# Performance work log

Measured on AMD Instinct MI355X. Metric: run time of the kernel, lower is better.

The kernel has to match this reference:

```python
import jax, jax.numpy as jnp
import numpy as np

NA, NP_, E = 40000, 60000, 80000
D, H = 512, 8
DK = D // H
SQRT_DK = float(DK) ** 0.5


def setup_inputs() -> dict:
    key = jax.random.key(0)
    ks = list(jax.random.split(key, 20))
    it = iter(ks)

    def nrm(shape, scale=1.0):
        return jax.random.normal(next(it), shape, dtype=jnp.float32) * scale

    xav = (6.0 / (DK + DK)) ** 0.5  # xavier_uniform bound for (dk, dk)
    w_scale = D ** -0.5
    inp = {
        "h_author": nrm((NA, D)),
        "h_paper": nrm((NP_, D)),
        "writes_src": jax.random.randint(next(it), (E,), 0, NA, dtype=jnp.int32),
        "writes_dst": jax.random.randint(next(it), (E,), 0, NP_, dtype=jnp.int32),
        "cites_src": jax.random.randint(next(it), (E,), 0, NP_, dtype=jnp.int32),
        "cites_dst": jax.random.randint(next(it), (E,), 0, NP_, dtype=jnp.int32),
        "wb_src": jax.random.randint(next(it), (E,), 0, NP_, dtype=jnp.int32),
        "wb_dst": jax.random.randint(next(it), (E,), 0, NA, dtype=jnp.int32),
        # per-node-type linear weights (2 types: 0=author, 1=paper)
        "Wk": nrm((2, D, D), w_scale), "bk": jnp.zeros((2, D), jnp.float32),
        "Wq": nrm((2, D, D), w_scale), "bq": jnp.zeros((2, D), jnp.float32),
        "Wv": nrm((2, D, D), w_scale), "bv": jnp.zeros((2, D), jnp.float32),
        "Wa": nrm((2, D, D), w_scale), "ba": jnp.zeros((2, D), jnp.float32),
        # per-relation params (3 relations: 0=writes, 1=cites, 2=written_by)
        "rel_att": jax.random.uniform(next(it), (3, H, DK, DK), jnp.float32, -xav, xav),
        "rel_msg": jax.random.uniform(next(it), (3, H, DK, DK), jnp.float32, -xav, xav),
        "rel_pri": jnp.ones((3, H), jnp.float32),
        "skip": jnp.ones((2,), jnp.float32),
    }
    return inp


def _edge_attn_agg(k, q, v, src, dst, pri, n_dst):
    # k, v: (N_src, H, DK) relation-transformed; q: (N_dst, H, DK)
    s = jnp.einsum('ehd,ehd->eh', q[dst], k[src]) * pri / SQRT_DK  # (E, H)
    m = jax.ops.segment_max(s, dst, num_segments=n_dst)            # edge softmax by dst
    ex = jnp.exp(s - m[dst])
    den = jax.ops.segment_sum(ex, dst, num_segments=n_dst)
    a = ex / den[dst]
    return jax.ops.segment_sum(v[src] * a[:, :, None], dst, num_segments=n_dst)


def reference(h_author, h_paper, writes_src, writes_dst, cites_src, cites_dst,
              wb_src, wb_dst, Wk, bk, Wq, bq, Wv, bv, Wa, ba,
              rel_att, rel_msg, rel_pri, skip):
    def proj(h, W, b, t):
        return (h @ W[t] + b[t]).reshape(-1, H, DK)

    k_a, v_a, q_a = proj(h_author, Wk, bk, 0), proj(h_author, Wv, bv, 0), proj(h_author, Wq, bq, 0)
    k_p, v_p, q_p = proj(h_paper, Wk, bk, 1), proj(h_paper, Wv, bv, 1), proj(h_paper, Wq, bq, 1)

    def rel(k, v, r):
        return (jnp.einsum('nhd,hde->nhe', k, rel_att[r]),
                jnp.einsum('nhd,hde->nhe', v, rel_msg[r]))

    k0, v0 = rel(k_a, v_a, 0)  # writes: author -> paper
    agg_w = _edge_attn_agg(k0, q_p, v0, writes_src, writes_dst, rel_pri[0], NP_)
    k1, v1 = rel(k_p, v_p, 1)  # cites: paper -> paper
    agg_c = _edge_attn_agg(k1, q_p, v1, cites_src, cites_dst, rel_pri[1], NP_)
    k2, v2 = rel(k_p, v_p, 2)  # written_by: paper -> author
    agg_b = _edge_attn_agg(k2, q_a, v2, wb_src, wb_dst, rel_pri[2], NA)

    t_paper = ((agg_w + agg_c) * 0.5).reshape(NP_, D)  # cross_reducer='mean'
    t_author = agg_b.reshape(NA, D)

    alpha = jax.nn.sigmoid(skip)
    out_a = (t_author @ Wa[0] + ba[0]) * alpha[0] + h_author * (1.0 - alpha[0])
    out_p = (t_paper @ Wa[1] + ba[1]) * alpha[1] + h_paper * (1.0 - alpha[1])
    return out_a, out_p
```

## Files before the change

kernel.cpp:

```cpp
#include <hip/hip_runtime.h>
#include <math.h>

#define D_ 512
#define H_ 8

typedef short bf16x8 __attribute__((ext_vector_type(8)));
typedef float f32x4 __attribute__((ext_vector_type(4)));

__device__ __forceinline__ unsigned short f2bf(float x) {
  unsigned int u = __float_as_uint(x);
  unsigned int r = (u + 0x7fff + ((u >> 16) & 1)) >> 16;
  return (unsigned short)r;
}
__device__ __forceinline__ float bf2f(unsigned short b) {
  return __uint_as_float(((unsigned int)b) << 16);
}

struct PrepArgs {
  const float *hA, *hP;
  unsigned short *hA16, *hP16;
  const float *fWin[6], *fbin[6], *frel[6];
  unsigned short *fWf[6];
  float *fbf[6];
  const float *tW[4];
  unsigned short *tWt[4];
  const float *cin[2];
  float *cout[2];
  int *degree;
  int NT;
  int b1, b2, b3, b4, b5;
};

__global__ __launch_bounds__(512) void prep_kernel(PrepArgs p) {
  const int b = blockIdx.x, t = threadIdx.x;
  if (b < p.b2) {
    const float* in; unsigned short* out; long i;
    if (b < p.b1) { in = p.hA; out = p.hA16; i = (long)b * 512 + t; }
    else          { in = p.hP; out = p.hP16; i = (long)(b - p.b1) * 512 + t; }
    float4 a = ((const float4*)in)[i * 2];
    float4 c = ((const float4*)in)[i * 2 + 1];
    bf16x8 o;
    o[0] = (short)f2bf(a.x); o[1] = (short)f2bf(a.y);
    o[2] = (short)f2bf(a.z); o[3] = (short)f2bf(a.w);
    o[4] = (short)f2bf(c.x); o[5] = (short)f2bf(c.y);
    o[6] = (short)f2bf(c.z); o[7] = (short)f2bf(c.w);
    ((bf16x8*)out)[i] = o;
  } else if (b < p.b3) {
    int idx = b - p.b2;
    int job = idx / 513, row = idx - job * 513;
    int h = t >> 6, e = t & 63;
    const float* src = (row < D_) ? (p.fWin[job] + (long)row * D_) : p.fbin[job];
    const float* rl = p.frel[job] + h * 64 * 64;
    float acc = 0.f;
#pragma unroll 16
    for (int d = 0; d < 64; ++d)
      acc = fmaf(src[h * 64 + d], rl[d * 64 + e], acc);
    if (row < D_) p.fWf[job][(long)t * D_ + row] = f2bf(acc);
    else p.fbf[job][t] = acc;
  } else if (b < p.b4) {
    int idx = b - p.b3;
    int job = idx >> 9, n = idx & 511;
    p.tWt[job][(long)n * D_ + t] = f2bf(p.tW[job][(long)t * D_ + n]);
  } else if (b < p.b5) {
    int job = b - p.b4;
    p.cout[job][t] = p.cin[job][t];
  } else {
    int i = (b - p.b5) * 512 + t;
    if (i < p.NT) p.degree[i] = 0;
  }
}

__global__ void hist_kernel(const int* __restrict__ w_dst,
                            const int* __restrict__ c_dst,
                            const int* __restrict__ b_dst,
                            int* __restrict__ degree, int E, int NP) {
  int i = blockIdx.x * blockDim.x + threadIdx.x;
  if (i >= 3 * E) return;
  int r = i / E, e = i - r * E;
  int d, base;
  if (r == 0)      { d = w_dst[e]; base = 0; }
  else if (r == 1) { d = c_dst[e]; base = NP; }
  else             { d = b_dst[e]; base = 2 * NP; }
  atomicAdd(degree + base + d, 1);
}

__global__ void scan1_kernel(const int* __restrict__ in, int* __restrict__ out,
                             int* __restrict__ aux, int n) {
  __shared__ int tmp[256];
  int t = threadIdx.x;
  int i = blockIdx.x * 256 + t;
  int v = (i < n) ? in[i] : 0;
  tmp[t] = v;
  __syncthreads();
#pragma unroll
  for (int d = 1; d < 256; d <<= 1) {
    int add = (t >= d) ? tmp[t - d] : 0;
    __syncthreads();
    tmp[t] += add;
    __syncthreads();
  }
  if (i < n) out[i] = tmp[t] - v;
  if (t == 255) aux[blockIdx.x] = tmp[255];
}

__global__ void scan2_kernel(int* __restrict__ aux, int nb) {
  __shared__ int tmp[1024];
  int t = threadIdx.x;
  int v = (t < nb) ? aux[t] : 0;
  tmp[t] = v;
  __syncthreads();
#pragma unroll
  for (int d = 1; d < 1024; d <<= 1) {
    int add = (t >= d) ? tmp[t - d] : 0;
    __syncthreads();
    tmp[t] += add;
    __syncthreads();
  }
  if (t < nb) aux[t] = tmp[t] - v;
}

__global__ void scan3_kernel(int* __restrict__ starts, int* __restrict__ cursor,
                             const int* __restrict__ aux, int n) {
  int i = blockIdx.x * 256 + threadIdx.x;
  if (i >= n) return;
  int s = starts[i] + aux[blockIdx.x];
  starts[i] = s;
  cursor[i] = s;
}

__global__ void scatter_kernel(const int* __restrict__ w_src, const int* __restrict__ w_dst,
                               const int* __restrict__ c_src, const int* __restrict__ c_dst,
                               const int* __restrict__ b_src, const int* __restrict__ b_dst,
                               int* __restrict__ cursor, int* __restrict__ csr,
                               int E, int NP) {
  int i = blockIdx.x * blockDim.x + threadIdx.x;
  if (i >= 3 * E) return;
  int r = i / E, e = i - r * E;
  int s, d, base;
  if (r == 0)      { s = w_src[e]; d = w_dst[e]; base = 0; }
  else if (r == 1) { s = c_src[e]; d = c_dst[e]; base = NP; }
  else             { s = b_src[e]; d = b_dst[e]; base = 2 * NP; }
  int pos = atomicAdd(cursor + base + d, 1);
  csr[pos] = s;
}

__global__ __launch_bounds__(256) void attn_all(
    const unsigned short* __restrict__ Pq,
    const unsigned short* __restrict__ Akw, const unsigned short* __restrict__ Avw,
    const unsigned short* __restrict__ Pkc, const unsigned short* __restrict__ Pvc,
    const unsigned short* __restrict__ Aq,
    const unsigned short* __restrict__ Pkb, const unsigned short* __restrict__ Pvb,
    const int* __restrict__ csr, const int* __restrict__ starts,
    const int* __restrict__ degree, const float* __restrict__ pri,
    unsigned short* __restrict__ t16, int NP, int NA, int NAp) {
  long gid = (long)blockIdx.x * blockDim.x + threadIdx.x;
  int gw = (int)(gid >> 6);
  if (gw >= NP + NAp) return;
  int lane = threadIdx.x & 63;
  int h = lane >> 3, off = (lane & 7) << 3;

  const unsigned short* q;
  long orow;
  int node;
  const int paper = gw < NP;
  if (paper) {
    node = gw; q = Pq;
    orow = (long)(NAp + node) * D_ + h * 64 + off;
  } else {
    int aw = gw - NP;
    orow = (long)aw * D_ + h * 64 + off;
    if (aw >= NA) {
      bf16x8 z;
#pragma unroll
      for (int r = 0; r < 8; ++r) z[r] = 0;
      *(bf16x8*)(t16 + orow) = z;
      return;
    }
    node = aw; q = Aq;
  }

  bf16x8 qv = *(const bf16x8*)(q + (long)node * D_ + h * 64 + off);
  float qf[8];
#pragma unroll
  for (int r = 0; r < 8; ++r) qf[r] = bf2f((unsigned short)qv[r]);

  float res[8] = {};

  auto process = [&](const unsigned short* K, const unsigned short* V,
                     int nodeabs, float ps) {
    int st = starts[nodeabs], dg = degree[nodeabs];
    float m = -INFINITY, l = 0.f;
    float acc[8] = {};
    for (int i = 0; i < dg; ++i) {
      int s = csr[st + i];
      const long ro = (long)s * D_ + h * 64 + off;
      bf16x8 kv = *(const bf16x8*)(K + ro);
      bf16x8 vv = *(const bf16x8*)(V + ro);
      float dot = 0.f;
#pragma unroll
      for (int r = 0; r < 8; ++r)
        dot = fmaf(qf[r], bf2f((unsigned short)kv[r]), dot);
      dot += __shfl_xor(dot, 1);
      dot += __shfl_xor(dot, 2);
      dot += __shfl_xor(dot, 4);
      float sc = dot * ps;
      float mn = fmaxf(m, sc);
      float scale = __expf(m - mn);
      float pv = __expf(sc - mn);
      l = l * scale + pv;
#pragma unroll
      for (int r = 0; r < 8; ++r)
        acc[r] = acc[r] * scale + pv * bf2f((unsigned short)vv[r]);
      m = mn;
    }
    if (l > 0.f) {
      float inv = 1.f / l;
#pragma unroll
      for (int r = 0; r < 8; ++r) res[r] += acc[r] * inv;
    }
  };

  float outscale;
  if (paper) {
    process(Akw, Avw, node, pri[h] * 0.125f);
    process(Pkc, Pvc, NP + node, pri[8 + h] * 0.125f);
    outscale = 0.5f;
  } else {
    process(Pkb, Pvb, 2 * NP + node, pri[16 + h] * 0.125f);
    outscale = 1.0f;
  }

  bf16x8 o;
#pragma unroll
  for (int r = 0; r < 8; ++r) o[r] = (short)f2bf(res[r] * outscale);
  *(bf16x8*)(t16 + orow) = o;
}

__device__ __forceinline__ void gload_lds16(const void* g, void* l) {
  __builtin_amdgcn_global_load_lds(
      (const __attribute__((address_space(1))) void*)g,
      (__attribute__((address_space(3))) void*)l, 16, 0, 0);
}

struct ProjArgs {
  const unsigned short *A0, *A1;
  const unsigned short *B0, *B1;
  const float *bias0, *bias1;
  void* outs[8];
  int M0, M1, split;
};

__global__ __launch_bounds__(512, 2) void gemm_proj(ProjArgs pa) {
  __shared__ unsigned short Asm[2][256 * 64];
  __shared__ unsigned short Bsm[2][256 * 64];

  const int nwg = gridDim.x, orig = blockIdx.x;
  const int q8 = nwg >> 3, r8 = nwg & 7;
  const int xcd = orig & 7, pos = orig >> 3;
  const int wgid =
      (xcd < r8 ? xcd * (q8 + 1) : r8 * (q8 + 1) + (xcd - r8) * q8) + pos;

  int reg, mt, nt;
  if (wgid < pa.split) { reg = 0; mt = wgid / 6; nt = wgid - mt * 6; }
  else { int r = wgid - pa.split; reg = 1; mt = r / 10; nt = r - mt * 10; }
  const unsigned short* A  = reg ? pa.A1 : pa.A0;
  const unsigned short* Bt = reg ? pa.B1 : pa.B0;
  const float* bias = reg ? pa.bias1 : pa.bias0;
  const int M = reg ? pa.M1 : pa.M0;
  const int bm = mt * 256, bn = nt * 256;

  const int tid = threadIdx.x;
  const int wave = tid >> 6, lane = tid & 63;
  const int wm = (wave >> 2) * 128;
  const int wn = (wave & 3) * 64;
  const int srow = tid >> 3;
  const int swz = ((tid & 7) ^ (srow & 7)) * 8;

  f32x4 acc[8][4] = {};
  const int rr = lane & 15;
  const int rx = (rr & 7) << 4;

  auto STAGE = [&](int buf, int kt) {
    const int k0 = kt * 64;
#pragma unroll
    for (int i = 0; i < 4; ++i) {
      int gr = bm + srow + i * 64;
      if (gr >= M) gr = M - 1;
      gload_lds16(A + (long)gr * D_ + k0 + swz, &Asm[buf][i * 4096 + wave * 512]);
    }
#pragma unroll
    for (int i = 0; i < 4; ++i) {
      int gr = bn + srow + i * 64;
      gload_lds16(Bt + (long)gr * D_ + k0 + swz, &Bsm[buf][i * 4096 + wave * 512]);
    }
  };

  STAGE(0, 0);
  STAGE(1, 1);
#pragma unroll
  for (int t = 0; t < 8; ++t) {
    const int p = t & 1;
    if (t == 7) asm volatile("s_waitcnt vmcnt(0)" ::: "memory");
    else        asm volatile("s_waitcnt vmcnt(8)" ::: "memory");
    __builtin_amdgcn_s_barrier();
    asm volatile("" ::: "memory");

#pragma unroll
    for (int kk = 0; kk < 2; ++kk) {
      const int cb = kk * 64 + (lane >> 4) * 16;
      const int cs = cb ^ rx;
      bf16x8 af[8], bfr[4];
#pragma unroll
      for (int mi = 0; mi < 8; ++mi)
        af[mi] = *(const bf16x8*)((const char*)&Asm[p][0] +
                                  (wm + mi * 16 + rr) * 128 + cs);
#pragma unroll
      for (int nj = 0; nj < 4; ++nj)
        bfr[nj] = *(const bf16x8*)((const char*)&Bsm[p][0] +
                                   (wn + nj * 16 + rr) * 128 + cs);
      __builtin_amdgcn_s_setprio(1);
#pragma unroll
      for (int mi = 0; mi < 8; ++mi)
#pragma unroll
        for (int nj = 0; nj < 4; ++nj)
          acc[mi][nj] = __builtin_amdgcn_mfma_f32_16x16x32_bf16(
              af[mi], bfr[nj], acc[mi][nj], 0, 0, 0);
      __builtin_amdgcn_s_setprio(0);
    }

    asm volatile("" ::: "memory");
    __builtin_amdgcn_s_barrier();
    asm volatile("" ::: "memory");
    if (t + 2 < 8) STAGE(p, t + 2);
  }

  const int cr = (lane >> 4) * 4;
  const int cc = lane & 15;
  const int matu = (bn + wn) >> 9;
  const int wcb = (bn + wn) & 511;
  unsigned short* ob16 = (unsigned short*)pa.outs[(reg ? 3 : 0) + matu];
#pragma unroll
  for (int mi = 0; mi < 8; ++mi) {
    int rowb = bm + wm + mi * 16 + cr;
#pragma unroll
    for (int nj = 0; nj < 4; ++nj) {
      int col = bn + wn + nj * 16 + cc;
      float bb = bias[col];
#pragma unroll
      for (int r = 0; r < 4; ++r) {
        int row = rowb + r;
        if (row >= M) continue;
        float val = acc[mi][nj][r] + bb;
        ob16[(long)row * D_ + wcb + nj * 16 + cc] = f2bf(val);
      }
    }
  }
}

struct OutArgs {
  const unsigned short* A;
  const unsigned short *B0, *B1;
  const float *bias0, *bias1;
  const float *H0, *H1;
  const float* skip;
  float *o0, *o1;
  int mtsplit, NAp, M0, M1;
};

__global__ __launch_bounds__(512, 2) void gemm_out(OutArgs oa) {
  __shared__ unsigned short Asm[2][256 * 64];
  __shared__ unsigned short Bsm[2][256 * 64];

  const int nwg = gridDim.x, orig = blockIdx.x;
  const int q8 = nwg >> 3, r8 = nwg & 7;
  const int xcd = orig & 7, pos = orig >> 3;
  const int wgid =
      (xcd < r8 ? xcd * (q8 + 1) : r8 * (q8 + 1) + (xcd - r8) * q8) + pos;

  const int bmt = wgid >> 1;
  const int bn = (wgid & 1) * 256;
  const int reg = bmt >= oa.mtsplit;
  const int bm = (reg ? bmt - oa.mtsplit : bmt) * 256;
  const int abase = reg ? oa.NAp : 0;
  const int M = reg ? oa.M1 : oa.M0;
  const unsigned short* Bt = reg ? oa.B1 : oa.B0;
  const float* bias = reg ? oa.bias1 : oa.bias0;
  const float* Hres = reg ? oa.H1 : oa.H0;
  float* outp = reg ? oa.o1 : oa.o0;

  const int tid = threadIdx.x;
  const int wave = tid >> 6, lane = tid & 63;
  const int wm = (wave >> 2) * 128;
  const int wn = (wave & 3) * 64;
  const int srow = tid >> 3;
  const int swz = ((tid & 7) ^ (srow & 7)) * 8;

  f32x4 acc[8][4] = {};
  const int rr = lane & 15;
  const int rx = (rr & 7) << 4;

  auto STAGE = [&](int buf, int kt) {
    const int k0 = kt * 64;
#pragma unroll
    for (int i = 0; i < 4; ++i) {
      int gr = bm + srow + i * 64;
      if (gr >= M) gr = M - 1;
      gload_lds16(oa.A + (long)(abase + gr) * D_ + k0 + swz,
                  &Asm[buf][i * 4096 + wave * 512]);
    }
#pragma unroll
    for (int i = 0; i < 4; ++i) {
      int gr = bn + srow + i * 64;
      gload_lds16(Bt + (long)gr * D_ + k0 + swz,
                  &Bsm[buf][i * 4096 + wave * 512]);
    }
  };

  STAGE(0, 0);
  STAGE(1, 1);
#pragma unroll
  for (int t = 0; t < 8; ++t) {
    const int p = t & 1;
    if (t == 7) asm volatile("s_waitcnt vmcnt(0)" ::: "memory");
    else        asm volatile("s_waitcnt vmcnt(8)" ::: "memory");
    __builtin_amdgcn_s_barrier();
    asm volatile("" ::: "memory");

#pragma unroll
    for (int kk = 0; kk < 2; ++kk) {
      const int cb = kk * 64 + (lane >> 4) * 16;
      const int cs = cb ^ rx;
      bf16x8 af[8], bfr[4];
#pragma unroll
      for (int mi = 0; mi < 8; ++mi)
        af[mi] = *(const bf16x8*)((const char*)&Asm[p][0] +
                                  (wm + mi * 16 + rr) * 128 + cs);
#pragma unroll
      for (int nj = 0; nj < 4; ++nj)
        bfr[nj] = *(const bf16x8*)((const char*)&Bsm[p][0] +
                                   (wn + nj * 16 + rr) * 128 + cs);
      __builtin_amdgcn_s_setprio(1);
#pragma unroll
      for (int mi = 0; mi < 8; ++mi)
#pragma unroll
        for (int nj = 0; nj < 4; ++nj)
          acc[mi][nj] = __builtin_amdgcn_mfma_f32_16x16x32_bf16(
              af[mi], bfr[nj], acc[mi][nj], 0, 0, 0);
      __builtin_amdgcn_s_setprio(0);
    }

    asm volatile("" ::: "memory");
    __builtin_amdgcn_s_barrier();
    asm volatile("" ::: "memory");
    if (t + 2 < 8) STAGE(p, t + 2);
  }

  float sv = oa.skip[reg];
  float alpha = 1.f / (1.f + expf(-sv));
  float beta = 1.f - alpha;
  const int cr = (lane >> 4) * 4;
  const int cc = lane & 15;
#pragma unroll
  for (int mi = 0; mi < 8; ++mi) {
    int rowb = bm + wm + mi * 16 + cr;
#pragma unroll
    for (int nj = 0; nj < 4; ++nj) {
      int col = bn + wn + nj * 16 + cc;
      float bb = bias[col];
#pragma unroll
      for (int r = 0; r < 4; ++r) {
        int row = rowb + r;
        if (row >= M) continue;
        float val = acc[mi][nj][r] + bb;
        val = val * alpha + Hres[(long)row * D_ + col] * beta;
        outp[(long)row * D_ + col] = val;
      }
    }
  }
}

extern "C" void kernel_launch(void* const* d_in, const int* in_sizes, int n_in,
                              void* d_out, int out_size, void* d_ws, size_t ws_size,
                              hipStream_t stream) {
  const float* h_author = (const float*)d_in[0];
  const float* h_paper  = (const float*)d_in[1];
  const int* w_src = (const int*)d_in[2];
  const int* w_dst = (const int*)d_in[3];
  const int* c_src = (const int*)d_in[4];
  const int* c_dst = (const int*)d_in[5];
  const int* b_src = (const int*)d_in[6];
  const int* b_dst = (const int*)d_in[7];
  const float* Wk = (const float*)d_in[8];
  const float* bk = (const float*)d_in[9];
  const float* Wq = (const float*)d_in[10];
  const float* bq = (const float*)d_in[11];
  const float* Wv = (const float*)d_in[12];
  const float* bv = (const float*)d_in[13];
  const float* Wa = (const float*)d_in[14];
  const float* ba = (const float*)d_in[15];
  const float* rel_att = (const float*)d_in[16];
  const float* rel_msg = (const float*)d_in[17];
  const float* rel_pri = (const float*)d_in[18];
  const float* skip = (const float*)d_in[19];

  const int NA = in_sizes[0] / D_;
  const int NP = in_sizes[1] / D_;
  const int E  = in_sizes[2];
  const int NT = 2 * NP + NA;
  const int tA = (NA + 255) / 256;
  const int tP = (NP + 255) / 256;
  const int NAp = tA * 256;

  char* w = (char*)d_ws;
  auto alloc = [&](long bytes) {
    char* p = w;
    w += (bytes + 255) & ~255L;
    return p;
  };
  unsigned short* hA16 = (unsigned short*)alloc((long)NA * D_ * 2);
  unsigned short* hP16 = (unsigned short*)alloc((long)NP * D_ * 2);
  unsigned short* Pq   = (unsigned short*)alloc((long)NP * D_ * 2);
  unsigned short* Pkc  = (unsigned short*)alloc((long)NP * D_ * 2);
  unsigned short* Pvc  = (unsigned short*)alloc((long)NP * D_ * 2);
  unsigned short* Pkb  = (unsigned short*)alloc((long)NP * D_ * 2);
  unsigned short* Pvb  = (unsigned short*)alloc((long)NP * D_ * 2);
  unsigned short* Aq   = (unsigned short*)alloc((long)NA * D_ * 2);
  unsigned short* Akw  = (unsigned short*)alloc((long)NA * D_ * 2);
  unsigned short* Avw  = (unsigned short*)alloc((long)NA * D_ * 2);
  unsigned short* t16  = (unsigned short*)alloc((long)(NAp + NP) * D_ * 2);
  unsigned short* BtP  = (unsigned short*)alloc((long)2560 * D_ * 2);
  unsigned short* BtA  = (unsigned short*)alloc((long)1536 * D_ * 2);
  float* bfP           = (float*)alloc(2560 * 4);
  float* bfA           = (float*)alloc(1536 * 4);
  unsigned short* Wa0t = (unsigned short*)alloc((long)D_ * D_ * 2);
  unsigned short* Wa1t = (unsigned short*)alloc((long)D_ * D_ * 2);
  int* degree          = (int*)alloc((long)NT * 4);
  int* starts          = (int*)alloc((long)NT * 4);
  int* cursor          = (int*)alloc((long)NT * 4);
  int* csr             = (int*)alloc((long)3 * E * 4);
  int* aux             = (int*)alloc(((long)NT / 256 + 2) * 4);

  const long WD = (long)D_ * D_;
  const long RS = (long)H_ * 64 * 64;
  const long SEG = (long)D_ * D_;

  float* out_a = (float*)d_out;
  float* out_p = out_a + (long)NA * D_;

  {
    PrepArgs p;
    p.hA = h_author; p.hP = h_paper; p.hA16 = hA16; p.hP16 = hP16;
    p.fWin[0] = Wk + WD; p.fbin[0] = bk + D_; p.frel[0] = rel_att + RS;
    p.fWf[0] = BtP + SEG;     p.fbf[0] = bfP + 512;
    p.fWin[1] = Wv + WD; p.fbin[1] = bv + D_; p.frel[1] = rel_msg + RS;
    p.fWf[1] = BtP + 2 * SEG; p.fbf[1] = bfP + 1024;
    p.fWin[2] = Wk + WD; p.fbin[2] = bk + D_; p.frel[2] = rel_att + 2 * RS;
    p.fWf[2] = BtP + 3 * SEG; p.fbf[2] = bfP + 1536;
    p.fWin[3] = Wv + WD; p.fbin[3] = bv + D_; p.frel[3] = rel_msg + 2 * RS;
    p.fWf[3] = BtP + 4 * SEG; p.fbf[3] = bfP + 2048;
    p.fWin[4] = Wk;      p.fbin[4] = bk;      p.frel[4] = rel_att;
    p.fWf[4] = BtA + SEG;     p.fbf[4] = bfA + 512;
    p.fWin[5] = Wv;      p.fbin[5] = bv;      p.frel[5] = rel_msg;
    p.fWf[5] = BtA + 2 * SEG; p.fbf[5] = bfA + 1024;
    p.tW[0] = Wq + WD; p.tWt[0] = BtP;
    p.tW[1] = Wq;      p.tWt[1] = BtA;
    p.tW[2] = Wa;      p.tWt[2] = Wa0t;
    p.tW[3] = Wa + WD; p.tWt[3] = Wa1t;
    p.cin[0] = bq + D_; p.cout[0] = bfP;
    p.cin[1] = bq;      p.cout[1] = bfA;
    p.degree = degree; p.NT = NT;
    p.b1 = NA / 8;
    p.b2 = p.b1 + NP / 8;
    p.b3 = p.b2 + 6 * 513;
    p.b4 = p.b3 + 4 * 512;
    p.b5 = p.b4 + 2;
    int total = p.b5 + (NT + 511) / 512;
    prep_kernel<<<total, 512, 0, stream>>>(p);
  }

  {
    int th = 3 * E;
    hist_kernel<<<(th + 255) / 256, 256, 0, stream>>>(w_dst, c_dst, b_dst,
                                                      degree, E, NP);
    int nb = (NT + 255) / 256;
    scan1_kernel<<<nb, 256, 0, stream>>>(degree, starts, aux, NT);
    scan2_kernel<<<1, 1024, 0, stream>>>(aux, nb);
    scan3_kernel<<<nb, 256, 0, stream>>>(starts, cursor, aux, NT);
    scatter_kernel<<<(th + 255) / 256, 256, 0, stream>>>(
        w_src, w_dst, c_src, c_dst, b_src, b_dst, cursor, csr, E, NP);
  }

  {
    ProjArgs pa;
    pa.A0 = hA16; pa.A1 = hP16;
    pa.B0 = BtA;  pa.B1 = BtP;
    pa.bias0 = bfA; pa.bias1 = bfP;
    pa.outs[0] = Aq;  pa.outs[1] = Akw; pa.outs[2] = Avw;
    pa.outs[3] = Pq;  pa.outs[4] = Pkc; pa.outs[5] = Pvc;
    pa.outs[6] = Pkb; pa.outs[7] = Pvb;
    pa.M0 = NA; pa.M1 = NP;
    pa.split = tA * 6;
    int nwg = pa.split + tP * 10;
    gemm_proj<<<nwg, 512, 0, stream>>>(pa);
  }

  {
    long th = (long)(NP + NAp) * 64;
    attn_all<<<(int)((th + 255) / 256), 256, 0, stream>>>(
        Pq, Akw, Avw, Pkc, Pvc, Aq, Pkb, Pvb,
        csr, starts, degree, rel_pri, t16, NP, NA, NAp);
  }

  {
    OutArgs oa;
    oa.A = t16;
    oa.B0 = Wa0t; oa.B1 = Wa1t;
    oa.bias0 = ba; oa.bias1 = ba + D_;
    oa.H0 = h_author; oa.H1 = h_paper;
    oa.skip = skip;
    oa.o0 = out_a; oa.o1 = out_p;
    oa.mtsplit = tA; oa.NAp = NAp; oa.M0 = NA; oa.M1 = NP;
    int nwg = (tA + tP) * 2;
    gemm_out<<<nwg, 512, 0, stream>>>(oa);
  }
}
```

Before: 919.0 us.

## Shrink GEMM tiles to 256x128 with triple-buffered LDS and split staging

Both GEMM kernels (projection and output) now use 256x128 tiles instead of 256x256. Each wave computes a 64x64 sub-tile, which halves the accumulator registers. LDS staging goes from double to triple buffering, and each prefetch is split into two halves issued between the kk sub-steps, so global loads overlap the MFMA work more evenly. The launch grids double to match. The intent is better occupancy and latency hiding. The cost is more B-tile and A-tile re-reads across workgroups, plus an extra barrier per k-step.

```diff
diff --git a/kernel.cpp b/kernel.cpp
--- a/kernel.cpp
+++ b/kernel.cpp
@@ -250,113 +250,6 @@
   int M0, M1, split;
 };
 
-__global__ __launch_bounds__(512, 2) void gemm_proj(ProjArgs pa) {
-  __shared__ unsigned short Asm[2][256 * 64];
-  __shared__ unsigned short Bsm[2][256 * 64];
-
-  const int nwg = gridDim.x, orig = blockIdx.x;
-  const int q8 = nwg >> 3, r8 = nwg & 7;
-  const int xcd = orig & 7, pos = orig >> 3;
-  const int wgid =
-      (xcd < r8 ? xcd * (q8 + 1) : r8 * (q8 + 1) + (xcd - r8) * q8) + pos;
-
-  int reg, mt, nt;
-  if (wgid < pa.split) { reg = 0; mt = wgid / 6; nt = wgid - mt * 6; }
-  else { int r = wgid - pa.split; reg = 1; mt = r / 10; nt = r - mt * 10; }
-  const unsigned short* A  = reg ? pa.A1 : pa.A0;
-  const unsigned short* Bt = reg ? pa.B1 : pa.B0;
-  const float* bias = reg ? pa.bias1 : pa.bias0;
-  const int M = reg ? pa.M1 : pa.M0;
-  const int bm = mt * 256, bn = nt * 256;
-
-  const int tid = threadIdx.x;
-  const int wave = tid >> 6, lane = tid & 63;
-  const int wm = (wave >> 2) * 128;
-  const int wn = (wave & 3) * 64;
-  const int srow = tid >> 3;
-  const int swz = ((tid & 7) ^ (srow & 7)) * 8;
-
-  f32x4 acc[8][4] = {};
-  const int rr = lane & 15;
-  const int rx = (rr & 7) << 4;
-
-  auto STAGE = [&](int buf, int kt) {
-    const int k0 = kt * 64;
-#pragma unroll
-    for (int i = 0; i < 4; ++i) {
-      int gr = bm + srow + i * 64;
-      if (gr >= M) gr = M - 1;
-      gload_lds16(A + (long)gr * D_ + k0 + swz, &Asm[buf][i * 4096 + wave * 512]);
-    }
-#pragma unroll
-    for (int i = 0; i < 4; ++i) {
-      int gr = bn + srow + i * 64;
-      gload_lds16(Bt + (long)gr * D_ + k0 + swz, &Bsm[buf][i * 4096 + wave * 512]);
-    }
-  };
-
-  STAGE(0, 0);
-  STAGE(1, 1);
-#pragma unroll
-  for (int t = 0; t < 8; ++t) {
-    const int p = t & 1;
-    if (t == 7) asm volatile("s_waitcnt vmcnt(0)" ::: "memory");
-    else        asm volatile("s_waitcnt vmcnt(8)" ::: "memory");
-    __builtin_amdgcn_s_barrier();
-    asm volatile("" ::: "memory");
-
-#pragma unroll
-    for (int kk = 0; kk < 2; ++kk) {
-      const int cb = kk * 64 + (lane >> 4) * 16;
-      const int cs = cb ^ rx;
-      bf16x8 af[8], bfr[4];
-#pragma unroll
-      for (int mi = 0; mi < 8; ++mi)
-        af[mi] = *(const bf16x8*)((const char*)&Asm[p][0] +
-                                  (wm + mi * 16 + rr) * 128 + cs);
-#pragma unroll
-      for (int nj = 0; nj < 4; ++nj)
-        bfr[nj] = *(const bf16x8*)((const char*)&Bsm[p][0] +
-                                   (wn + nj * 16 + rr) * 128 + cs);
-      __builtin_amdgcn_s_setprio(1);
-#pragma unroll
-      for (int mi = 0; mi < 8; ++mi)
-#pragma unroll
-        for (int nj = 0; nj < 4; ++nj)
-          acc[mi][nj] = __builtin_amdgcn_mfma_f32_16x16x32_bf16(
-              af[mi], bfr[nj], acc[mi][nj], 0, 0, 0);
-      __builtin_amdgcn_s_setprio(0);
-    }
-
-    asm volatile("" ::: "memory");
-    __builtin_amdgcn_s_barrier();
-    asm volatile("" ::: "memory");
-    if (t + 2 < 8) STAGE(p, t + 2);
-  }
-
-  const int cr = (lane >> 4) * 4;
-  const int cc = lane & 15;
-  const int matu = (bn + wn) >> 9;
-  const int wcb = (bn + wn) & 511;
-  unsigned short* ob16 = (unsigned short*)pa.outs[(reg ? 3 : 0) + matu];
-#pragma unroll
-  for (int mi = 0; mi < 8; ++mi) {
-    int rowb = bm + wm + mi * 16 + cr;
-#pragma unroll
-    for (int nj = 0; nj < 4; ++nj) {
-      int col = bn + wn + nj * 16 + cc;
-      float bb = bias[col];
-#pragma unroll
-      for (int r = 0; r < 4; ++r) {
-        int row = rowb + r;
-        if (row >= M) continue;
-        float val = acc[mi][nj][r] + bb;
-        ob16[(long)row * D_ + wcb + nj * 16 + cc] = f2bf(val);
-      }
-    }
-  }
-}
-
 struct OutArgs {
   const unsigned short* A;
   const unsigned short *B0, *B1;
@@ -367,9 +260,76 @@
   int mtsplit, NAp, M0, M1;
 };
 
-__global__ __launch_bounds__(512, 2) void gemm_out(OutArgs oa) {
-  __shared__ unsigned short Asm[2][256 * 64];
-  __shared__ unsigned short Bsm[2][256 * 64];
+#define GEMM_CORE(A_PTR, B_PTR)                                               \
+  f32x4 acc[4][4] = {};                                                       \
+  const int rr = lane & 15;                                                   \
+  const int rx = (rr & 7) << 4;                                               \
+  auto STAGE_PART = [&](int u, int part) {                                    \
+    const int sl = u % 3;                                                     \
+    const int k0 = u * 64 + swz;                                              \
+    if (part == 0) {                                                          \
+      _Pragma("unroll")                                                       \
+      for (int i = 0; i < 2; ++i) {                                           \
+        int gr = bm + srow + i * 64;                                          \
+        if (gr >= M) gr = M - 1;                                              \
+        gload_lds16((A_PTR) + (long)gr * D_ + k0,                             \
+                    &As[sl][i * 4096 + wave * 512]);                          \
+      }                                                                       \
+      int gb = bn + srow;                                                     \
+      gload_lds16((B_PTR) + (long)gb * D_ + k0, &Bs[sl][wave * 512]);         \
+    } else {                                                                  \
+      _Pragma("unroll")                                                       \
+      for (int i = 2; i < 4; ++i) {                                           \
+        int gr = bm + srow + i * 64;                                          \
+        if (gr >= M) gr = M - 1;                                              \
+        gload_lds16((A_PTR) + (long)gr * D_ + k0,                             \
+                    &As[sl][i * 4096 + wave * 512]);                          \
+      }                                                                       \
+      int gb = bn + 64 + srow;                                                \
+      gload_lds16((B_PTR) + (long)gb * D_ + k0, &Bs[sl][4096 + wave * 512]);  \
+    }                                                                         \
+  };                                                                          \
+  STAGE_PART(0, 0); STAGE_PART(0, 1);                                         \
+  STAGE_PART(1, 0); STAGE_PART(1, 1);                                         \
+  _Pragma("unroll")                                                           \
+  for (int t = 0; t < 8; ++t) {                                               \
+    if (t < 7) asm volatile("s_waitcnt vmcnt(6)" ::: "memory");               \
+    else       asm volatile("s_waitcnt vmcnt(0)" ::: "memory");               \
+    __builtin_amdgcn_s_barrier();                                             \
+    asm volatile("" ::: "memory");                                            \
+    const int sslot = t % 3;                                                  \
+    const char* ab = (const char*)&As[sslot][0];                              \
+    const char* bb = (const char*)&Bs[sslot][0];                              \
+    _Pragma("unroll")                                                         \
+    for (int kk = 0; kk < 2; ++kk) {                                          \
+      const int cs = (kk * 64 + (lane >> 4) * 16) ^ rx;                       \
+      bf16x8 af[4], bfr[4];                                                   \
+      _Pragma("unroll")                                                       \
+      for (int mi = 0; mi < 4; ++mi)                                          \
+        af[mi] = *(const bf16x8*)(ab + (wm + mi * 16 + rr) * 128 + cs);       \
+      _Pragma("unroll")                                                       \
+      for (int nj = 0; nj < 4; ++nj)                                          \
+        bfr[nj] = *(const bf16x8*)(bb + (wn + nj * 16 + rr) * 128 + cs);      \
+      if (t < 6) STAGE_PART(t + 2, kk);                                       \
+      __builtin_amdgcn_s_setprio(1);                                          \
+      _Pragma("unroll")                                                       \
+      for (int mi = 0; mi < 4; ++mi)                                          \
+        _Pragma("unroll")                                                     \
+        for (int nj = 0; nj < 4; ++nj)                                        \
+          acc[mi][nj] = __builtin_amdgcn_mfma_f32_16x16x32_bf16(              \
+              af[mi], bfr[nj], acc[mi][nj], 0, 0, 0);                         \
+      __builtin_amdgcn_s_setprio(0);                                          \
+      asm volatile("" ::: "memory");                                          \
+      if (kk == 0) {                                                          \
+        __builtin_amdgcn_s_barrier();                                         \
+        asm volatile("" ::: "memory");                                        \
+      }                                                                       \
+    }                                                                         \
+  }
+
+__global__ __launch_bounds__(512, 2) void gemm_proj(ProjArgs pa) {
+  __shared__ unsigned short As[3][256 * 64];
+  __shared__ unsigned short Bs[3][128 * 64];
 
   const int nwg = gridDim.x, orig = blockIdx.x;
   const int q8 = nwg >> 3, r8 = nwg & 7;
@@ -377,12 +337,62 @@
   const int wgid =
       (xcd < r8 ? xcd * (q8 + 1) : r8 * (q8 + 1) + (xcd - r8) * q8) + pos;
 
-  const int bmt = wgid >> 1;
-  const int bn = (wgid & 1) * 256;
+  int reg, mt, nt;
+  if (wgid < pa.split) { reg = 0; mt = wgid / 12; nt = wgid - mt * 12; }
+  else { int r = wgid - pa.split; reg = 1; mt = r / 20; nt = r - mt * 20; }
+  const unsigned short* A  = reg ? pa.A1 : pa.A0;
+  const unsigned short* Bt = reg ? pa.B1 : pa.B0;
+  const float* bias = reg ? pa.bias1 : pa.bias0;
+  const int M = reg ? pa.M1 : pa.M0;
+  const int bm = mt * 256, bn = nt * 128;
+
+  const int tid = threadIdx.x;
+  const int wave = tid >> 6, lane = tid & 63;
+  const int wm = (wave >> 1) * 64;
+  const int wn = (wave & 1) * 64;
+  const int srow = tid >> 3;
+  const int swz = ((tid & 7) ^ (srow & 7)) * 8;
+
+  GEMM_CORE(A, Bt)
+
+  const int cr = (lane >> 4) * 4;
+  const int cc = lane & 15;
+  const int matu = (bn + wn) >> 9;
+  const int wcb = (bn + wn) & 511;
+  unsigned short* ob16 = (unsigned short*)pa.outs[(reg ? 3 : 0) + matu];
+#pragma unroll
+  for (int mi = 0; mi < 4; ++mi) {
+    int rowb = bm + wm + mi * 16 + cr;
+#pragma unroll
+    for (int nj = 0; nj < 4; ++nj) {
+      float bb = bias[bn + wn + nj * 16 + cc];
+#pragma unroll
+      for (int r = 0; r < 4; ++r) {
+        int row = rowb + r;
+        if (row >= M) continue;
+        ob16[(long)row * D_ + wcb + nj * 16 + cc] = f2bf(acc[mi][nj][r] + bb);
+      }
+    }
+  }
+}
+
+__global__ __launch_bounds__(512, 2) void gemm_out(OutArgs oa) {
+  __shared__ unsigned short As[3][256 * 64];
+  __shared__ unsigned short Bs[3][128 * 64];
+
+  const int nwg = gridDim.x, orig = blockIdx.x;
+  const int q8 = nwg >> 3, r8 = nwg & 7;
+  const int xcd = orig & 7, pos = orig >> 3;
+  const int wgid =
+      (xcd < r8 ? xcd * (q8 + 1) : r8 * (q8 + 1) + (xcd - r8) * q8) + pos;
+
+  const int bmt = wgid >> 2;
+  const int bn = (wgid & 3) * 128;
   const int reg = bmt >= oa.mtsplit;
   const int bm = (reg ? bmt - oa.mtsplit : bmt) * 256;
   const int abase = reg ? oa.NAp : 0;
   const int M = reg ? oa.M1 : oa.M0;
+  const unsigned short* Aeff = oa.A + (long)abase * D_;
   const unsigned short* Bt = reg ? oa.B1 : oa.B0;
   const float* bias = reg ? oa.bias1 : oa.bias0;
   const float* Hres = reg ? oa.H1 : oa.H0;
@@ -390,70 +400,12 @@
 
   const int tid = threadIdx.x;
   const int wave = tid >> 6, lane = tid & 63;
-  const int wm = (wave >> 2) * 128;
-  const int wn = (wave & 3) * 64;
+  const int wm = (wave >> 1) * 64;
+  const int wn = (wave & 1) * 64;
   const int srow = tid >> 3;
   const int swz = ((tid & 7) ^ (srow & 7)) * 8;
 
-  f32x4 acc[8][4] = {};
-  const int rr = lane & 15;
-  const int rx = (rr & 7) << 4;
-
-  auto STAGE = [&](int buf, int kt) {
-    const int k0 = kt * 64;
-#pragma unroll
-    for (int i = 0; i < 4; ++i) {
-      int gr = bm + srow + i * 64;
-      if (gr >= M) gr = M - 1;
-      gload_lds16(oa.A + (long)(abase + gr) * D_ + k0 + swz,
-                  &Asm[buf][i * 4096 + wave * 512]);
-    }
-#pragma unroll
-    for (int i = 0; i < 4; ++i) {
-      int gr = bn + srow + i * 64;
-      gload_lds16(Bt + (long)gr * D_ + k0 + swz,
-                  &Bsm[buf][i * 4096 + wave * 512]);
-    }
-  };
-
-  STAGE(0, 0);
-  STAGE(1, 1);
-#pragma unroll
-  for (int t = 0; t < 8; ++t) {
-    const int p = t & 1;
-    if (t == 7) asm volatile("s_waitcnt vmcnt(0)" ::: "memory");
-    else        asm volatile("s_waitcnt vmcnt(8)" ::: "memory");
-    __builtin_amdgcn_s_barrier();
-    asm volatile("" ::: "memory");
-
-#pragma unroll
-    for (int kk = 0; kk < 2; ++kk) {
-      const int cb = kk * 64 + (lane >> 4) * 16;
-      const int cs = cb ^ rx;
-      bf16x8 af[8], bfr[4];
-#pragma unroll
-      for (int mi = 0; mi < 8; ++mi)
-        af[mi] = *(const bf16x8*)((const char*)&Asm[p][0] +
-                                  (wm + mi * 16 + rr) * 128 + cs);
-#pragma unroll
-      for (int nj = 0; nj < 4; ++nj)
-        bfr[nj] = *(const bf16x8*)((const char*)&Bsm[p][0] +
-                                   (wn + nj * 16 + rr) * 128 + cs);
-      __builtin_amdgcn_s_setprio(1);
-#pragma unroll
-      for (int mi = 0; mi < 8; ++mi)
-#pragma unroll
-        for (int nj = 0; nj < 4; ++nj)
-          acc[mi][nj] = __builtin_amdgcn_mfma_f32_16x16x32_bf16(
-              af[mi], bfr[nj], acc[mi][nj], 0, 0, 0);
-      __builtin_amdgcn_s_setprio(0);
-    }
-
-    asm volatile("" ::: "memory");
-    __builtin_amdgcn_s_barrier();
-    asm volatile("" ::: "memory");
-    if (t + 2 < 8) STAGE(p, t + 2);
-  }
+  GEMM_CORE(Aeff, Bt)
 
   float sv = oa.skip[reg];
   float alpha = 1.f / (1.f + expf(-sv));
@@ -461,7 +413,7 @@
   const int cr = (lane >> 4) * 4;
   const int cc = lane & 15;
 #pragma unroll
-  for (int mi = 0; mi < 8; ++mi) {
+  for (int mi = 0; mi < 4; ++mi) {
     int rowb = bm + wm + mi * 16 + cr;
 #pragma unroll
     for (int nj = 0; nj < 4; ++nj) {
@@ -599,8 +551,8 @@
     pa.outs[3] = Pq;  pa.outs[4] = Pkc; pa.outs[5] = Pvc;
     pa.outs[6] = Pkb; pa.outs[7] = Pvb;
     pa.M0 = NA; pa.M1 = NP;
-    pa.split = tA * 6;
-    int nwg = pa.split + tP * 10;
+    pa.split = tA * 12;
+    int nwg = pa.split + tP * 20;
     gemm_proj<<<nwg, 512, 0, stream>>>(pa);
   }
 
@@ -620,7 +572,7 @@
     oa.skip = skip;
     oa.o0 = out_a; oa.o1 = out_p;
     oa.mtsplit = tA; oa.NAp = NAp; oa.M0 = NA; oa.M1 = NP;
-    int nwg = (tA + tP) * 2;
+    int nwg = (tA + tP) * 4;
     gemm_out<<<nwg, 512, 0, stream>>>(oa);
   }
 }
```

Result: slower. 954.3 us (+3.8%).
